# Optimization experiments

Hardware: AMD Instinct MI355X
Metric: run time of the kernel (lower is better)

Reference implementation:

```python
import jax, jax.numpy as jnp
import numpy as np

N, E, C, O, H, W, K = 32, 512, 64, 128, 64, 64, 3


def setup_inputs() -> dict:
    key = jax.random.key(0)
    k1, k2, k3, k4, k5, k6 = jax.random.split(key, 6)
    scale_w = 1.0 / np.sqrt(E)
    return {
        "embedding": jax.random.normal(k1, (N, E), dtype=jnp.float32),
        "images": jax.random.normal(k2, (N, C, H, W), dtype=jnp.float32),
        "w_weight": jax.random.uniform(k3, (O * C * K * K, E), dtype=jnp.float32, minval=-scale_w, maxval=scale_w),
        "w_bias": jax.random.uniform(k4, (O * C * K * K,), dtype=jnp.float32, minval=-scale_w, maxval=scale_w),
        "b_weight": jax.random.uniform(k5, (O, E), dtype=jnp.float32, minval=-scale_w, maxval=scale_w),
        "b_bias": jax.random.uniform(k6, (O,), dtype=jnp.float32, minval=-scale_w, maxval=scale_w),
    }


def reference(embedding, images, w_weight, w_bias, b_weight, b_bias):
    n, c, h, w = images.shape
    o = b_bias.shape[0]
    # per-sample generated filters and biases
    c1_w = embedding @ w_weight.T + w_bias          # [N, O*C*K*K]
    c1_b = embedding @ b_weight.T + b_bias          # [N, O]
    filt = c1_w.reshape(n, o, c, K, K)              # matches torch view(O, C*K*K)
    # im2col equivalent: pad then gather 3x3 shifted views -> [N,C,K,K,H,W]
    xp = jnp.pad(images, ((0, 0), (0, 0), (1, 1), (1, 1)))
    patches = jnp.stack(
        [xp[:, :, i:i + h, j:j + w] for i in range(K) for j in range(K)], axis=2
    ).reshape(n, c, K, K, h, w)
    out = jnp.einsum('nocij,ncijhw->nohw', filt, patches)
    return out + c1_b[:, :, None, None]
```

## Files before the change

kernel.cpp:

```cpp
#include <hip/hip_runtime.h>
#include <hip/hip_bf16.h>

#define N_  32
#define E_  512
#define C_  64
#define O_  128
#define H_  64
#define W_  64
#define CK9 576
#define M_  (O_*CK9)
#define IMGP_ROWB 9216

typedef __bf16 bf16x8 __attribute__((ext_vector_type(8)));
typedef __bf16 bf16x4 __attribute__((ext_vector_type(4)));
typedef float  f32x4  __attribute__((ext_vector_type(4)));

__device__ __forceinline__ void gload_lds16(const void* g, void* l) {
    typedef __attribute__((address_space(1))) const void gvoid;
    typedef __attribute__((address_space(3))) void lvoid;
    __builtin_amdgcn_global_load_lds((gvoid*)g, (lvoid*)l, 16, 0, 0);
}

__global__ __launch_bounds__(256, 4) void producers(
    const float* __restrict__ emb, const float* __restrict__ img,
    const float* __restrict__ w_weight, const float* __restrict__ w_bias,
    const float* __restrict__ b_weight, const float* __restrict__ b_bias,
    __bf16* __restrict__ filt, __bf16* __restrict__ imgp, float* __restrict__ c1b)
{
    __shared__ __align__(16) char smem[33280];
    int bid = blockIdx.x;
    int tid = threadIdx.x;

    if (bid < 576) {
        __bf16* embS = (__bf16*)smem;
        int wave = tid >> 6, lane = tid & 63;
        int quad = lane >> 4, l16 = lane & 15;
        int m0 = bid * 128;

#pragma unroll
        for (int i = 0; i < 16; i++) {
            int idx = (i * 256 + tid) * 4;
            int n = idx >> 9, e = idx & 511;
            f32x4 v = *reinterpret_cast<const f32x4*>(emb + n * 512 + e);
            bf16x4 b;
            b[0] = (__bf16)v[0]; b[1] = (__bf16)v[1]; b[2] = (__bf16)v[2]; b[3] = (__bf16)v[3];
            *reinterpret_cast<bf16x4*>(&embS[n * 520 + e]) = b;
        }
        __syncthreads();

        const float* a0p = w_weight + (size_t)(m0 + wave * 32 + l16) * 512 + quad * 8;
        const float* a1p = a0p + 16 * 512;

        f32x4 acc[2][2];
#pragma unroll
        for (int mi = 0; mi < 2; mi++)
#pragma unroll
            for (int ni = 0; ni < 2; ni++)
                acc[mi][ni] = (f32x4){0.f, 0.f, 0.f, 0.f};

#pragma unroll
        for (int kk = 0; kk < 16; kk++) {
            int k0 = kk * 32;
            f32x4 v00 = *reinterpret_cast<const f32x4*>(a0p + k0);
            f32x4 v01 = *reinterpret_cast<const f32x4*>(a0p + k0 + 4);
            f32x4 v10 = *reinterpret_cast<const f32x4*>(a1p + k0);
            f32x4 v11 = *reinterpret_cast<const f32x4*>(a1p + k0 + 4);
            bf16x8 a0, a1;
            a0[0] = (__bf16)v00[0]; a0[1] = (__bf16)v00[1];
            a0[2] = (__bf16)v00[2]; a0[3] = (__bf16)v00[3];
            a0[4] = (__bf16)v01[0]; a0[5] = (__bf16)v01[1];
            a0[6] = (__bf16)v01[2]; a0[7] = (__bf16)v01[3];
            a1[0] = (__bf16)v10[0]; a1[1] = (__bf16)v10[1];
            a1[2] = (__bf16)v10[2]; a1[3] = (__bf16)v10[3];
            a1[4] = (__bf16)v11[0]; a1[5] = (__bf16)v11[1];
            a1[6] = (__bf16)v11[2]; a1[7] = (__bf16)v11[3];
            bf16x8 b0 = *reinterpret_cast<const bf16x8*>(&embS[l16 * 520 + k0 + quad * 8]);
            bf16x8 b1 = *reinterpret_cast<const bf16x8*>(&embS[(16 + l16) * 520 + k0 + quad * 8]);
            acc[0][0] = __builtin_amdgcn_mfma_f32_16x16x32_bf16(a0, b0, acc[0][0], 0, 0, 0);
            acc[0][1] = __builtin_amdgcn_mfma_f32_16x16x32_bf16(a0, b1, acc[0][1], 0, 0, 0);
            acc[1][0] = __builtin_amdgcn_mfma_f32_16x16x32_bf16(a1, b0, acc[1][0], 0, 0, 0);
            acc[1][1] = __builtin_amdgcn_mfma_f32_16x16x32_bf16(a1, b1, acc[1][1], 0, 0, 0);
        }

#pragma unroll
        for (int mi = 0; mi < 2; mi++) {
#pragma unroll
            for (int r = 0; r < 4; r++) {
                int m = m0 + wave * 32 + mi * 16 + quad * 4 + r;
                int o = m / 576;
                int rem = m - o * 576;
                int c = rem / 9;
                int t = rem - c * 9;
                int kp = t * 64 + c;
                size_t base = ((size_t)(kp >> 3) << 10) + ((size_t)o << 3) + (kp & 7);
                float bias = w_bias[m];
#pragma unroll
                for (int ni = 0; ni < 2; ni++) {
                    int n = ni * 16 + l16;
                    filt[(size_t)n * M_ + base] = (__bf16)(acc[mi][ni][r] + bias);
                }
            }
        }
    } else if (bid < 2688) {
        __bf16* ldsT = (__bf16*)smem;
        int blk = bid - 576;
        int n = blk / 66, hh = blk - n * 66;
        char* dst = (char*)imgp + ((size_t)n * 66 + hh) * IMGP_ROWB;

        bf16x8 zero = {(__bf16)0.f, (__bf16)0.f, (__bf16)0.f, (__bf16)0.f,
                       (__bf16)0.f, (__bf16)0.f, (__bf16)0.f, (__bf16)0.f};

        if (hh == 0 || hh == 65) {
#pragma unroll
            for (int j = 0; j < 3; j++) {
                int u = j * 256 + tid;
                if (u < 576) *reinterpret_cast<bf16x8*>(dst + u * 16) = zero;
            }
            return;
        }

        int h = hh - 1;
        const float* srcn = img + (size_t)n * (C_ * H_ * W_) + h * 64;
        int c0 = (tid & 15) * 4, w0 = (tid >> 4) * 4;
#pragma unroll
        for (int i = 0; i < 4; i++) {
            f32x4 v = *reinterpret_cast<const f32x4*>(srcn + (size_t)(c0 + i) * 4096 + w0);
#pragma unroll
            for (int j = 0; j < 4; j++)
                ldsT[(w0 + j) * 72 + c0 + i] = (__bf16)v[j];
        }
        __syncthreads();

#pragma unroll
        for (int j = 0; j < 3; j++) {
            int u = j * 256 + tid;
            if (u < 576) {
                int col = u >> 3, s = u & 7;
                bf16x8 val = zero;
                if (col >= 1 && col <= 64) {
                    int b = s ^ (col & 7);
                    val = *reinterpret_cast<const bf16x8*>(&ldsT[(col - 1) * 72 + b * 8]);
                }
                *reinterpret_cast<bf16x8*>(dst + u * 16) = val;
            }
        }
    } else {
        int wave = tid >> 6, lane = tid & 63;
        int wid = ((bid - 2688) << 2) + wave;
        int n = wid >> 7, o = wid & 127;
        const float* e = emb + (size_t)n * E_ + lane * 8;
        const float* b = b_weight + (size_t)o * E_ + lane * 8;
        f32x4 e0 = *reinterpret_cast<const f32x4*>(e);
        f32x4 e1 = *reinterpret_cast<const f32x4*>(e + 4);
        f32x4 w0 = *reinterpret_cast<const f32x4*>(b);
        f32x4 w1 = *reinterpret_cast<const f32x4*>(b + 4);
        float s = e0[0]*w0[0] + e0[1]*w0[1] + e0[2]*w0[2] + e0[3]*w0[3]
                + e1[0]*w1[0] + e1[1]*w1[1] + e1[2]*w1[2] + e1[3]*w1[3];
#pragma unroll
        for (int off = 32; off; off >>= 1) s += __shfl_xor(s, off, 64);
        if (lane == 0) c1b[wid] = s + b_bias[o];
    }
}

__global__ __launch_bounds__(256, 4) void conv_gemm(
    const __bf16* __restrict__ imgp, const __bf16* __restrict__ filt,
    const float* __restrict__ c1b, float* __restrict__ out)
{
    __shared__ __align__(16) char smemc[36864];
    float* ep    = (float*)smemc;
    char*  slabB = smemc;

    int tid  = threadIdx.x;
    int wave = tid >> 6, lane = tid & 63;
    int quad = lane >> 4, l16 = lane & 15;

    int blk = blockIdx.x;
    int n  = ((blk & 7) << 2) + ((blk >> 3) & 3);
    int pt = blk >> 5;
    int h0 = pt * 2;

    const __bf16* fN   = filt + (size_t)n * M_;
    const char*   srcN = (const char*)imgp + (size_t)n * 66 * IMGP_ROWB;
    int oB = wave * 32 + l16;

    float biasv[2][4];
#pragma unroll
    for (int mi = 0; mi < 2; mi++)
#pragma unroll
        for (int r = 0; r < 4; r++)
            biasv[mi][r] = c1b[(n << 7) + wave * 32 + mi * 16 + quad * 4 + r];

    const char* src = srcN + (size_t)h0 * IMGP_ROWB;
#pragma unroll
    for (int j = 0; j < 9; j++)
        gload_lds16(src + (j * 256 + tid) * 16,
                    slabB + (j * 256 + wave * 64) * 16);

    int colA[4][3][2];
#pragma unroll
    for (int cb = 0; cb < 4; cb++)
#pragma unroll
        for (int tj = 0; tj < 3; tj++) {
            int col = cb * 16 + l16 + tj;
#pragma unroll
            for (int ck = 0; ck < 2; ck++)
                colA[cb][tj][ck] = col * 128 + (((quad + ck * 4) ^ (col & 7)) << 4);
        }

    f32x4 acc[2][8];
#pragma unroll
    for (int mi = 0; mi < 2; mi++)
#pragma unroll
        for (int ni = 0; ni < 8; ni++)
            acc[mi][ni] = (f32x4){0.f, 0.f, 0.f, 0.f};

    __syncthreads();

#pragma unroll
    for (int tj = 0; tj < 3; tj++) {
#pragma unroll
        for (int ck = 0; ck < 2; ck++) {
            bf16x8 aR2[2][3];
#pragma unroll
            for (int mi = 0; mi < 2; mi++)
#pragma unroll
                for (int di = 0; di < 3; di++) {
                    int kk = 2 * (di * 3 + tj) + ck;
                    aR2[mi][di] = *reinterpret_cast<const bf16x8*>(
                        fN + (((kk * 4 + quad) << 10) + ((oB + mi * 16) << 3)));
                }
            bf16x8 b2[4][4];
#pragma unroll
            for (int row = 0; row < 4; row++)
#pragma unroll
                for (int cb = 0; cb < 4; cb++)
                    b2[row][cb] = *reinterpret_cast<const bf16x8*>(
                        slabB + row * IMGP_ROWB + colA[cb][tj][ck]);
#pragma unroll
            for (int di = 0; di < 3; di++)
#pragma unroll
                for (int mi = 0; mi < 2; mi++)
#pragma unroll
                    for (int lh = 0; lh < 2; lh++)
#pragma unroll
                        for (int cb = 0; cb < 4; cb++)
                            acc[mi][(lh << 2) | cb] = __builtin_amdgcn_mfma_f32_16x16x32_bf16(
                                aR2[mi][di], b2[lh + di][cb], acc[mi][(lh << 2) | cb], 0, 0, 0);
        }
    }

#pragma unroll
    for (int mi = 0; mi < 2; mi++) {
        __syncthreads();
#pragma unroll
        for (int ni = 0; ni < 8; ni++) {
            int lh = ni >> 2, cb = ni & 3;
#pragma unroll
            for (int r = 0; r < 4; r++)
                ep[wave * 2112 + (quad * 4 + r) * 132 + lh * 64 + cb * 16 + l16] =
                    acc[mi][ni][r] + biasv[mi][r];
        }
        __syncthreads();
#pragma unroll
        for (int u = 0; u < 8; u++) {
            int idx = u * 256 + tid;
            int row = idx >> 5, s16 = idx & 31;
            int w2 = row >> 4, ol = row & 15;
            f32x4 v = *reinterpret_cast<const f32x4*>(&ep[w2 * 2112 + ol * 132 + s16 * 4]);
            int o = w2 * 32 + mi * 16 + ol;
            *reinterpret_cast<f32x4*>(
                out + (((size_t)(n << 7) + o) << 12) + (pt << 7) + s16 * 4) = v;
        }
    }
}

extern "C" void kernel_launch(void* const* d_in, const int* in_sizes, int n_in,
                              void* d_out, int out_size, void* d_ws, size_t ws_size,
                              hipStream_t stream)
{
    (void)in_sizes; (void)n_in; (void)out_size; (void)ws_size;
    const float* emb      = (const float*)d_in[0];
    const float* images   = (const float*)d_in[1];
    const float* w_weight = (const float*)d_in[2];
    const float* w_bias   = (const float*)d_in[3];
    const float* b_weight = (const float*)d_in[4];
    const float* b_bias   = (const float*)d_in[5];
    float* out = (float*)d_out;

    __bf16* filt = (__bf16*)d_ws;
    float*  c1b  = (float*)((char*)d_ws + (size_t)N_ * M_ * 2);
    __bf16* imgp = (__bf16*)((char*)d_ws + (size_t)N_ * M_ * 2 + 16384);

    producers<<<dim3(3712), dim3(256), 0, stream>>>(
        emb, images, w_weight, w_bias, b_weight, b_bias, filt, imgp, c1b);
    conv_gemm<<<dim3(1024), dim3(256), 0, stream>>>(imgp, filt, c1b, out);
}
```

Baseline: 317.3 us.

## Split producer kernel and stage filter-weight loads through LDS via global_load_lds

The fused producer kernel is split into a dedicated filter-generation kernel and a smaller kernel for image packing and bias dot products, with different occupancy bounds. The filter GEMM now streams w_weight tiles into a swizzled LDS slab using direct global-to-LDS loads instead of strided per-lane global reads, giving coalesced 16-byte accesses. This adds an extra kernel launch, two barriers per K step with no double buffering, and serializes the packing work behind the filter GEMM.

```diff
diff --git a/kernel.cpp b/kernel.cpp
--- a/kernel.cpp
+++ b/kernel.cpp
@@ -21,90 +21,114 @@
     __builtin_amdgcn_global_load_lds((gvoid*)g, (lvoid*)l, 16, 0, 0);
 }
 
-__global__ __launch_bounds__(256, 4) void producers(
+__global__ __launch_bounds__(256, 4) void gen_filters(
+    const float* __restrict__ emb, const float* __restrict__ w_weight,
+    const float* __restrict__ w_bias, __bf16* __restrict__ filt)
+{
+    __shared__ __align__(16) char smem[49664];
+    __bf16* embS = (__bf16*)smem;
+    char*   slab = smem + 33280;
+
+    int tid  = threadIdx.x;
+    int wave = tid >> 6, lane = tid & 63;
+    int quad = lane >> 4, l16 = lane & 15;
+    int m0 = blockIdx.x * 128;
+
+    const float* gbase = w_weight + (size_t)(m0 + (tid >> 3)) * 512
+                       + (((tid & 7) ^ ((tid >> 3) & 7)) << 2);
+    char* ldst = slab + wave * 1024;
+
+#pragma unroll
+    for (int j = 0; j < 4; j++)
+        gload_lds16(gbase + (size_t)j * 32 * 512, ldst + j * 4096);
+
+#pragma unroll
+    for (int i = 0; i < 16; i++) {
+        int idx = (i * 256 + tid) * 4;
+        int n = idx >> 9, e = idx & 511;
+        f32x4 v = *reinterpret_cast<const f32x4*>(emb + n * 512 + e);
+        bf16x4 b;
+        b[0] = (__bf16)v[0]; b[1] = (__bf16)v[1]; b[2] = (__bf16)v[2]; b[3] = (__bf16)v[3];
+        *reinterpret_cast<bf16x4*>(&embS[n * 520 + e]) = b;
+    }
+
+    char* pr0 = slab + (wave * 32 + l16) * 128;
+    char* pr1 = pr0 + 16 * 128;
+    int sA = (((2 * quad)     ^ (l16 & 7)) << 4);
+    int sB = (((2 * quad + 1) ^ (l16 & 7)) << 4);
+
+    f32x4 acc[2][2];
+#pragma unroll
+    for (int mi = 0; mi < 2; mi++)
+#pragma unroll
+        for (int ni = 0; ni < 2; ni++)
+            acc[mi][ni] = (f32x4){0.f, 0.f, 0.f, 0.f};
+
+#pragma unroll
+    for (int kk = 0; kk < 16; kk++) {
+        __syncthreads();
+
+        f32x4 v00 = *reinterpret_cast<const f32x4*>(pr0 + sA);
+        f32x4 v01 = *reinterpret_cast<const f32x4*>(pr0 + sB);
+        f32x4 v10 = *reinterpret_cast<const f32x4*>(pr1 + sA);
+        f32x4 v11 = *reinterpret_cast<const f32x4*>(pr1 + sB);
+        bf16x8 a0, a1;
+        a0[0] = (__bf16)v00[0]; a0[1] = (__bf16)v00[1];
+        a0[2] = (__bf16)v00[2]; a0[3] = (__bf16)v00[3];
+        a0[4] = (__bf16)v01[0]; a0[5] = (__bf16)v01[1];
+        a0[6] = (__bf16)v01[2]; a0[7] = (__bf16)v01[3];
+        a1[0] = (__bf16)v10[0]; a1[1] = (__bf16)v10[1];
+        a1[2] = (__bf16)v10[2]; a1[3] = (__bf16)v10[3];
+        a1[4] = (__bf16)v11[0]; a1[5] = (__bf16)v11[1];
+        a1[6] = (__bf16)v11[2]; a1[7] = (__bf16)v11[3];
+        bf16x8 b0 = *reinterpret_cast<const bf16x8*>(&embS[l16 * 520 + kk * 32 + quad * 8]);
+        bf16x8 b1 = *reinterpret_cast<const bf16x8*>(&embS[(16 + l16) * 520 + kk * 32 + quad * 8]);
+        acc[0][0] = __builtin_amdgcn_mfma_f32_16x16x32_bf16(a0, b0, acc[0][0], 0, 0, 0);
+        acc[0][1] = __builtin_amdgcn_mfma_f32_16x16x32_bf16(a0, b1, acc[0][1], 0, 0, 0);
+        acc[1][0] = __builtin_amdgcn_mfma_f32_16x16x32_bf16(a1, b0, acc[1][0], 0, 0, 0);
+        acc[1][1] = __builtin_amdgcn_mfma_f32_16x16x32_bf16(a1, b1, acc[1][1], 0, 0, 0);
+
+        if (kk < 15) {
+            __syncthreads();
+#pragma unroll
+            for (int j = 0; j < 4; j++)
+                gload_lds16(gbase + (size_t)j * 32 * 512 + (kk + 1) * 32,
+                            ldst + j * 4096);
+        }
+    }
+
+#pragma unroll
+    for (int mi = 0; mi < 2; mi++) {
+#pragma unroll
+        for (int r = 0; r < 4; r++) {
+            int m = m0 + wave * 32 + mi * 16 + quad * 4 + r;
+            int o = m / 576;
+            int rem = m - o * 576;
+            int c = rem / 9;
+            int t = rem - c * 9;
+            int kp = t * 64 + c;
+            size_t base = ((size_t)(kp >> 3) << 10) + ((size_t)o << 3) + (kp & 7);
+            float bias = w_bias[m];
+#pragma unroll
+            for (int ni = 0; ni < 2; ni++) {
+                int n = ni * 16 + l16;
+                filt[(size_t)n * M_ + base] = (__bf16)(acc[mi][ni][r] + bias);
+            }
+        }
+    }
+}
+
+__global__ __launch_bounds__(256, 8) void pack_small(
     const float* __restrict__ emb, const float* __restrict__ img,
-    const float* __restrict__ w_weight, const float* __restrict__ w_bias,
     const float* __restrict__ b_weight, const float* __restrict__ b_bias,
-    __bf16* __restrict__ filt, __bf16* __restrict__ imgp, float* __restrict__ c1b)
+    __bf16* __restrict__ imgp, float* __restrict__ c1b)
 {
-    __shared__ __align__(16) char smem[33280];
+    __shared__ __align__(16) __bf16 ldsT[64 * 72];
     int bid = blockIdx.x;
     int tid = threadIdx.x;
 
-    if (bid < 576) {
-        __bf16* embS = (__bf16*)smem;
-        int wave = tid >> 6, lane = tid & 63;
-        int quad = lane >> 4, l16 = lane & 15;
-        int m0 = bid * 128;
-
-#pragma unroll
-        for (int i = 0; i < 16; i++) {
-            int idx = (i * 256 + tid) * 4;
-            int n = idx >> 9, e = idx & 511;
-            f32x4 v = *reinterpret_cast<const f32x4*>(emb + n * 512 + e);
-            bf16x4 b;
-            b[0] = (__bf16)v[0]; b[1] = (__bf16)v[1]; b[2] = (__bf16)v[2]; b[3] = (__bf16)v[3];
-            *reinterpret_cast<bf16x4*>(&embS[n * 520 + e]) = b;
-        }
-        __syncthreads();
-
-        const float* a0p = w_weight + (size_t)(m0 + wave * 32 + l16) * 512 + quad * 8;
-        const float* a1p = a0p + 16 * 512;
-
-        f32x4 acc[2][2];
-#pragma unroll
-        for (int mi = 0; mi < 2; mi++)
-#pragma unroll
-            for (int ni = 0; ni < 2; ni++)
-                acc[mi][ni] = (f32x4){0.f, 0.f, 0.f, 0.f};
-
-#pragma unroll
-        for (int kk = 0; kk < 16; kk++) {
-            int k0 = kk * 32;
-            f32x4 v00 = *reinterpret_cast<const f32x4*>(a0p + k0);
-            f32x4 v01 = *reinterpret_cast<const f32x4*>(a0p + k0 + 4);
-            f32x4 v10 = *reinterpret_cast<const f32x4*>(a1p + k0);
-            f32x4 v11 = *reinterpret_cast<const f32x4*>(a1p + k0 + 4);
-            bf16x8 a0, a1;
-            a0[0] = (__bf16)v00[0]; a0[1] = (__bf16)v00[1];
-            a0[2] = (__bf16)v00[2]; a0[3] = (__bf16)v00[3];
-            a0[4] = (__bf16)v01[0]; a0[5] = (__bf16)v01[1];
-            a0[6] = (__bf16)v01[2]; a0[7] = (__bf16)v01[3];
-            a1[0] = (__bf16)v10[0]; a1[1] = (__bf16)v10[1];
-            a1[2] = (__bf16)v10[2]; a1[3] = (__bf16)v10[3];
-            a1[4] = (__bf16)v11[0]; a1[5] = (__bf16)v11[1];
-            a1[6] = (__bf16)v11[2]; a1[7] = (__bf16)v11[3];
-            bf16x8 b0 = *reinterpret_cast<const bf16x8*>(&embS[l16 * 520 + k0 + quad * 8]);
-            bf16x8 b1 = *reinterpret_cast<const bf16x8*>(&embS[(16 + l16) * 520 + k0 + quad * 8]);
-            acc[0][0] = __builtin_amdgcn_mfma_f32_16x16x32_bf16(a0, b0, acc[0][0], 0, 0, 0);
-            acc[0][1] = __builtin_amdgcn_mfma_f32_16x16x32_bf16(a0, b1, acc[0][1], 0, 0, 0);
-            acc[1][0] = __builtin_amdgcn_mfma_f32_16x16x32_bf16(a1, b0, acc[1][0], 0, 0, 0);
-            acc[1][1] = __builtin_amdgcn_mfma_f32_16x16x32_bf16(a1, b1, acc[1][1], 0, 0, 0);
-        }
-
-#pragma unroll
-        for (int mi = 0; mi < 2; mi++) {
-#pragma unroll
-            for (int r = 0; r < 4; r++) {
-                int m = m0 + wave * 32 + mi * 16 + quad * 4 + r;
-                int o = m / 576;
-                int rem = m - o * 576;
-                int c = rem / 9;
-                int t = rem - c * 9;
-                int kp = t * 64 + c;
-                size_t base = ((size_t)(kp >> 3) << 10) + ((size_t)o << 3) + (kp & 7);
-                float bias = w_bias[m];
-#pragma unroll
-                for (int ni = 0; ni < 2; ni++) {
-                    int n = ni * 16 + l16;
-                    filt[(size_t)n * M_ + base] = (__bf16)(acc[mi][ni][r] + bias);
-                }
-            }
-        }
-    } else if (bid < 2688) {
-        __bf16* ldsT = (__bf16*)smem;
-        int blk = bid - 576;
-        int n = blk / 66, hh = blk - n * 66;
+    if (bid < 2112) {
+        int n = bid / 66, hh = bid - n * 66;
         char* dst = (char*)imgp + ((size_t)n * 66 + hh) * IMGP_ROWB;
 
         bf16x8 zero = {(__bf16)0.f, (__bf16)0.f, (__bf16)0.f, (__bf16)0.f,
@@ -146,7 +170,7 @@
         }
     } else {
         int wave = tid >> 6, lane = tid & 63;
-        int wid = ((bid - 2688) << 2) + wave;
+        int wid = ((bid - 2112) << 2) + wave;
         int n = wid >> 7, o = wid & 127;
         const float* e = emb + (size_t)n * E_ + lane * 8;
         const float* b = b_weight + (size_t)o * E_ + lane * 8;
@@ -291,7 +315,7 @@
     float*  c1b  = (float*)((char*)d_ws + (size_t)N_ * M_ * 2);
     __bf16* imgp = (__bf16*)((char*)d_ws + (size_t)N_ * M_ * 2 + 16384);
 
-    producers<<<dim3(3712), dim3(256), 0, stream>>>(
-        emb, images, w_weight, w_bias, b_weight, b_bias, filt, imgp, c1b);
+    gen_filters<<<dim3(576), dim3(256), 0, stream>>>(emb, w_weight, w_bias, filt);
+    pack_small<<<dim3(3136), dim3(256), 0, stream>>>(emb, images, b_weight, b_bias, imgp, c1b);
     conv_gemm<<<dim3(1024), dim3(256), 0, stream>>>(imgp, filt, c1b, out);
 }
```

Result: no change. 313.3 us (-1.3%).
